# Kernel tuning notes

Measured on AMD Instinct MI355X. Metric: run time of the kernel, lower is better.

## Reference

```python
import jax, jax.numpy as jnp
from jax import lax
import numpy as np

BATCH = 8
FH, FW, A = 32, 256, 6            # feature map height/width, anchors per cell
TOTAL_ANCHORS = FH * FW * A       # 49152
PRE_NMS_TOPN = 2000
POST_NMS_TOPN = 300
NMS_IOU = 0.7
VARIANCES = np.array([0.1, 0.1, 0.2, 0.2], dtype=np.float32)


def _make_anchors():
    # Grid anchors, normalized [y1, x1, y2, x2], A scales/ratios per cell.
    cy = (np.arange(FH, dtype=np.float32) + 0.5) / FH
    cx = (np.arange(FW, dtype=np.float32) + 0.5) / FW
    sizes = np.array([0.02, 0.04, 0.08, 0.03, 0.06, 0.12], dtype=np.float32)  # A sizes
    ratios = np.array([1.0, 1.0, 1.0, 2.0, 0.5, 1.0], dtype=np.float32)
    h = sizes * np.sqrt(ratios)
    w = sizes / np.sqrt(ratios)
    CY, CX = np.meshgrid(cy, cx, indexing='ij')            # [FH, FW]
    CY = CY[:, :, None]; CX = CX[:, :, None]               # [FH, FW, 1]
    y1 = CY - 0.5 * h; x1 = CX - 0.5 * w
    y2 = CY + 0.5 * h; x2 = CX + 0.5 * w
    anc = np.stack([y1, x1, y2, x2], axis=-1).reshape(-1, 4)  # [TOTAL_ANCHORS, 4]
    return jnp.asarray(anc, dtype=jnp.float32)


def setup_inputs() -> dict:
    key = jax.random.key(0)
    k1, k2 = jax.random.split(key)
    rpn_bbox_deltas = jax.random.normal(k1, (BATCH, FH, FW, A * 4), dtype=jnp.float32)
    rpn_labels = jax.random.normal(k2, (BATCH, FH, FW, A), dtype=jnp.float32)
    return {
        'rpn_bbox_deltas': rpn_bbox_deltas,
        'rpn_labels': rpn_labels,
        'anchors': _make_anchors(),
    }


def _decode(anchors, deltas):
    # anchors [N,4] y1x1y2x2, deltas [B,N,4] (dy,dx,dh,dw)
    ah = anchors[:, 2] - anchors[:, 0]
    aw = anchors[:, 3] - anchors[:, 1]
    acy = anchors[:, 0] + 0.5 * ah
    acx = anchors[:, 1] + 0.5 * aw
    bh = jnp.exp(deltas[..., 2]) * ah
    bw = jnp.exp(deltas[..., 3]) * aw
    bcy = deltas[..., 0] * ah + acy
    bcx = deltas[..., 1] * aw + acx
    y1 = bcy - 0.5 * bh
    x1 = bcx - 0.5 * bw
    return jnp.stack([y1, x1, y1 + bh, x1 + bw], axis=-1)


def _pairwise_iou(boxes):
    # boxes [N,4] -> [N,N]
    y1, x1, y2, x2 = boxes[:, 0], boxes[:, 1], boxes[:, 2], boxes[:, 3]
    area = (y2 - y1) * (x2 - x1)
    iy1 = jnp.maximum(y1[:, None], y1[None, :])
    ix1 = jnp.maximum(x1[:, None], x1[None, :])
    iy2 = jnp.minimum(y2[:, None], y2[None, :])
    ix2 = jnp.minimum(x2[:, None], x2[None, :])
    inter = jnp.maximum(iy2 - iy1, 0.0) * jnp.maximum(ix2 - ix1, 0.0)
    union = area[:, None] + area[None, :] - inter
    return inter / jnp.maximum(union, 1e-8)


def _nms_single(boxes, scores):
    # boxes [P,4] sorted by score desc, scores [P] in [0,1]
    P = boxes.shape[0]
    ious = _pairwise_iou(boxes)
    idx = jnp.arange(P)

    def body(i, keep):
        sup = (ious[i] > NMS_IOU) & (idx > i) & keep[i]
        return keep & (~sup)

    keep = lax.fori_loop(0, P, body, jnp.ones((P,), dtype=bool))
    masked = jnp.where(keep, scores, -1.0)
    top_sc, top_idx = lax.top_k(masked, POST_NMS_TOPN)
    valid = top_sc >= 0.0
    out_boxes = jnp.clip(boxes[top_idx], 0.0, 1.0) * valid[:, None].astype(boxes.dtype)
    out_scores = jnp.where(valid, top_sc, 0.0)
    return out_boxes, out_scores


def reference(rpn_bbox_deltas, rpn_labels, anchors):
    B = rpn_bbox_deltas.shape[0]
    deltas = rpn_bbox_deltas.reshape(B, TOTAL_ANCHORS, 4)
    labels = jax.nn.softmax(rpn_labels, axis=-1).reshape(B, TOTAL_ANCHORS)
    deltas = deltas * jnp.asarray(VARIANCES)
    bboxes = _decode(anchors, deltas)                          # [B, N, 4]
    pre_scores, pre_idx = lax.top_k(labels, PRE_NMS_TOPN)      # [B, P]
    pre_boxes = jnp.take_along_axis(bboxes, pre_idx[:, :, None], axis=1)  # [B, P, 4]
    roi_boxes, roi_scores = jax.vmap(_nms_single)(pre_boxes, pre_scores)
    return (lax.stop_gradient(roi_boxes), lax.stop_gradient(roi_scores))
```

## Files before the change

kernel.cpp:

```cpp
#include <hip/hip_runtime.h>
#include <cstdint>
#include <cstddef>

#define BATCH 8
#define FHh   32
#define FWw   256
#define NA    6
#define NANCH (FHh * FWw * NA)
#define PRE_K 2000
#define POST_K 300
#define SEGS  192
#define CAND_CAP 4096
#define BIN_LO 0x3E2Au
#define SH_BASE 0x3E00u
#define SHBIN 512
#define RMAX_EP 20

typedef unsigned long long u64;

#define WS_SC   0
#define WS_HIST 1572864
#define WS_CAND 4194304
#define WS_CNT  7340032
#define WS_PB   7602176
#define WS_PS   7858176
#define WS_SUPP 8388608

__global__ __launch_bounds__(1024) void k_zero(uint4* __restrict__ hist4) {
    hist4[threadIdx.x] = make_uint4(0u, 0u, 0u, 0u);
}

__global__ void k_softhist(const float* __restrict__ labels, float* __restrict__ scores,
                           unsigned int* __restrict__ hist) {
    int pos = blockIdx.x * blockDim.x + threadIdx.x;
    if (pos >= BATCH * FHh * FWw) return;
    int b = pos / (FHh * FWw);
    const float2* in2 = (const float2*)(labels + (size_t)pos * NA);
    float v[NA];
    float2 p0 = in2[0], p1 = in2[1], p2 = in2[2];
    v[0] = p0.x; v[1] = p0.y; v[2] = p1.x; v[3] = p1.y; v[4] = p2.x; v[5] = p2.y;
    float m = v[0];
#pragma unroll
    for (int a = 1; a < NA; ++a) m = fmaxf(m, v[a]);
    float s = 0.0f;
#pragma unroll
    for (int a = 0; a < NA; ++a) { v[a] = expf(v[a] - m); s += v[a]; }
    float inv = 1.0f / s;
    float2* o2 = (float2*)(scores + (size_t)pos * NA);
    unsigned int* hb = hist + (size_t)b * SHBIN;
#pragma unroll
    for (int a = 0; a < NA; ++a) v[a] *= inv;
    o2[0] = make_float2(v[0], v[1]);
    o2[1] = make_float2(v[2], v[3]);
    o2[2] = make_float2(v[4], v[5]);
#pragma unroll
    for (int a = 0; a < NA; ++a) {
        unsigned int bin = __float_as_uint(v[a]) >> 16;
        if (bin >= BIN_LO) atomicAdd(&hb[bin - SH_BASE], 1u);
    }
}

__global__ __launch_bounds__(256) void k_gather(
        const float* __restrict__ scores, const unsigned int* __restrict__ hist,
        u64* __restrict__ cand, unsigned int* __restrict__ counts) {
    const int blk = blockIdx.x;
    const int b = blk / SEGS, kb = blk - b * SEGS;
    const int tid = threadIdx.x;
    const int lane = tid & 63, w = tid >> 6;
    __shared__ unsigned int s_wsum[4];
    __shared__ unsigned int s_cut;
    __shared__ unsigned int s_wcnt[4];

    const unsigned int* hb = hist + (size_t)b * SHBIN;
    const int base = SHBIN - 2 * (tid + 1);
    unsigned int hlo = hb[base], hhi = hb[base + 1];
    unsigned int s = hlo + hhi;
    unsigned int inc = s;
#pragma unroll
    for (int d = 1; d < 64; d <<= 1) {
        unsigned int v = __shfl_up(inc, d);
        if (lane >= d) inc += v;
    }
    if (lane == 63) s_wsum[w] = inc;
    __syncthreads();
    unsigned int woff = 0;
#pragma unroll
    for (int i = 0; i < 4; ++i) if (i < w) woff += s_wsum[i];
    unsigned int excl = woff + inc - s;
    if (excl < PRE_K && excl + s >= PRE_K) {
        unsigned int run = excl + hhi;
        s_cut = SH_BASE + (unsigned int)(run >= PRE_K ? base + 1 : base);
    }
    __syncthreads();
    const unsigned int cutr = s_cut;

    const int idx = kb * 256 + tid;
    const unsigned int bits = __float_as_uint(scores[(size_t)b * NANCH + idx]);
    const bool pass = (bits >> 16) >= cutr;
    const u64 m = __ballot(pass);
    if (lane == 0) s_wcnt[w] = (unsigned int)__popcll(m);
    __syncthreads();
    unsigned int pre = 0, tot = 0;
#pragma unroll
    for (int i = 0; i < 4; ++i) { unsigned int c = s_wcnt[i]; if (i < w) pre += c; tot += c; }
    if (pass) {
        unsigned int rank = pre + (unsigned int)__popcll(m & ((1ull << lane) - 1ull));
        cand[((size_t)b * SEGS + kb) * 256 + rank] =
            ((u64)bits << 32) | (unsigned int)(~idx);
    }
    if (tid == 0) counts[b * SEGS + kb] = tot;
}

__global__ __launch_bounds__(1024) void k_rankdec(
        const u64* __restrict__ cand, const unsigned int* __restrict__ counts,
        const unsigned int* __restrict__ hist,
        const float* __restrict__ deltas, const float* __restrict__ anchors,
        float4* __restrict__ pre_boxes, float* __restrict__ pre_scores) {
    const int b = blockIdx.x;
    const int tid = threadIdx.x;
    const int lane = tid & 63, wid = tid >> 6;
    __shared__ u64 grouped[CAND_CAP];
    __shared__ unsigned int cursor[CAND_CAP];
    __shared__ unsigned int sfx_lds[SHBIN];
    __shared__ unsigned int s_ws8[8];
    for (int i = tid; i < CAND_CAP; i += 1024) { grouped[i] = 0ull; cursor[i] = 0u; }

    unsigned int c = (tid < SHBIN) ? hist[(size_t)b * SHBIN + (SHBIN - 1 - tid)] : 0u;
    unsigned int inc = c;
#pragma unroll
    for (int d = 1; d < 64; d <<= 1) {
        unsigned int v = __shfl_up(inc, d);
        if (lane >= d) inc += v;
    }
    if (lane == 63 && wid < 8) s_ws8[wid] = inc;
    __syncthreads();
    if (tid < SHBIN) {
        unsigned int woff = 0;
#pragma unroll
        for (int i = 0; i < 8; ++i) if (i < wid) woff += s_ws8[i];
        sfx_lds[SHBIN - 1 - tid] = woff + inc - c;
    }
    __syncthreads();

    if (tid < SEGS) {
        unsigned int v = counts[b * SEGS + tid];
        const u64* seg = cand + ((size_t)b * SEGS + tid) * 256;
        for (unsigned int k = 0; k < v; ++k) {
            u64 key = seg[k];
            unsigned int bin = (unsigned int)(key >> 48) - SH_BASE;
            unsigned int g0 = sfx_lds[bin];
            unsigned int slot = g0 + atomicAdd(&cursor[g0], 1u);
            if (slot < CAND_CAP) grouped[slot] = key;
        }
    }
    __syncthreads();

    for (int p = tid; p < CAND_CAP; p += 1024) {
        u64 key = grouped[p];
        if (key == 0ull) continue;
        unsigned int bin = (unsigned int)(key >> 48) - SH_BASE;
        unsigned int g0 = sfx_lds[bin];
        unsigned int cg = cursor[g0];
        unsigned int rank = g0;
        unsigned int qe = g0 + cg; if (qe > CAND_CAP) qe = CAND_CAP;
        for (unsigned int q = g0; q < qe; ++q) rank += (grouped[q] > key);
        if (rank < PRE_K) {
            int idx = (int)(~(unsigned int)key);
            float score = __uint_as_float((unsigned int)(key >> 32));
            const float* anc = anchors + (size_t)idx * 4;
            const float* del = deltas + ((size_t)b * NANCH + idx) * 4;
            float a0 = anc[0], a1 = anc[1], a2 = anc[2], a3 = anc[3];
            float ah = a2 - a0, aw = a3 - a1;
            float acy = a0 + 0.5f * ah, acx = a1 + 0.5f * aw;
            float d0 = del[0] * 0.1f, d1 = del[1] * 0.1f;
            float d2 = del[2] * 0.2f, d3 = del[3] * 0.2f;
            float bh = expf(d2) * ah, bw = expf(d3) * aw;
            float bcy = d0 * ah + acy, bcx = d1 * aw + acx;
            float y1 = bcy - 0.5f * bh, x1 = bcx - 0.5f * bw;
            pre_boxes[(size_t)b * PRE_K + rank] = make_float4(y1, x1, y1 + bh, x1 + bw);
            pre_scores[(size_t)b * PRE_K + rank] = score;
        }
    }
}

__global__ __launch_bounds__(64) void k_iou(const float4* __restrict__ pre_boxes,
                                            u64* __restrict__ supp) {
    const int cb = blockIdx.x;
    const int rb = blockIdx.y;
    const int b  = blockIdx.z;
    const int lane = threadIdx.x;
    const int i = rb * 64 + lane;
    const int j0 = cb * 64;
    if (cb < rb) return;
    __shared__ float4 sbox[64];
    const float4* boxes = pre_boxes + (size_t)b * PRE_K;
    int j = j0 + lane;
    sbox[lane] = (j < PRE_K) ? boxes[j] : make_float4(0.f, 0.f, 0.f, 0.f);
    __syncthreads();
    if (i >= PRE_K) return;
    float4 bi = boxes[i];
    float area_i = (bi.z - bi.x) * (bi.w - bi.y);
    u64 bits = 0ull;
    const int tmax = (PRE_K - j0 < 64) ? (PRE_K - j0) : 64;
    for (int t = 0; t < tmax; ++t) {
        int jj = j0 + t;
        if (jj <= i) continue;
        float4 bj = sbox[t];
        float iy1 = fmaxf(bi.x, bj.x), ix1 = fmaxf(bi.y, bj.y);
        float iy2 = fminf(bi.z, bj.z), ix2 = fminf(bi.w, bj.w);
        float inter = fmaxf(iy2 - iy1, 0.0f) * fmaxf(ix2 - ix1, 0.0f);
        float area_j = (bj.z - bj.x) * (bj.w - bj.y);
        float uni = area_i + area_j - inter;
        float iou = inter / fmaxf(uni, 1e-8f);
        if (iou > 0.7f) bits |= (1ull << t);
    }
    supp[((size_t)b * PRE_K + i) * 32 + cb] = bits;
}

__device__ __forceinline__ u64 readlane64(u64 x, int ln) {
    unsigned int lo = __builtin_amdgcn_readlane((unsigned int)x, ln);
    unsigned int hi = __builtin_amdgcn_readlane((unsigned int)(x >> 32), ln);
    return ((u64)hi << 32) | (u64)lo;
}

template <int ROWS>
__device__ __forceinline__ u64 proc_epoch(const u64* __restrict__ bufp, int wi,
                                          int p, int w, u64& r0, u64& r1) {
    const u64 wmask = (w >= wi) ? ~0ull : 0ull;
    u64 acc = r0 | r1;
    u64 cur = ~(readlane64(acc, wi) | readlane64(acc, 32 + wi));
#pragma unroll
    for (int g = 0; g < ROWS / 16; ++g) {
        u64 ld[8];
#pragma unroll
        for (int k = 0; k < 8; ++k)
            ld[k] = bufp[(g * 16 + 2 * k + p) * 32 + w] & wmask;
        u64 t0 = (ld[0] | ld[1]) | (ld[2] | ld[3]);
        u64 t1 = (ld[4] | ld[5]) | (ld[6] | ld[7]);
        u64 tor = t0 | t1;
        u64 intra = readlane64(tor, wi) | readlane64(tor, 32 + wi);
        if (intra == 0ull) {
#pragma unroll
            for (int k = 0; k < 8; ++k) {
                int bitpos = g * 16 + 2 * k + p;
                u64 msk = ((cur >> bitpos) & 1ull) ? ~0ull : 0ull;
                if (k & 1) r1 |= ld[k] & msk; else r0 |= ld[k] & msk;
            }
        } else {
#pragma unroll
            for (int c = 0; c < 16; ++c) {
                const int pi = c & 1, k = c >> 1;
                if ((cur >> (g * 16 + c)) & 1ull) {
                    cur &= ~readlane64(ld[k], pi * 32 + wi);
                    u64 msk = (p == pi) ? ~0ull : 0ull;
                    if (k & 1) r1 |= ld[k] & msk; else r0 |= ld[k] & msk;
                }
            }
        }
    }
    return cur;
}

__device__ void fill_epoch(u64* __restrict__ dst, const float4* __restrict__ boxes,
                           int e, int l, int rows) {
    const int total = rows * 32;
    for (int idx = l; idx < total; idx += 64) {
        const int rl = idx >> 5, w = idx & 31;
        const int i = e * 64 + rl;
        const int j0 = w * 64;
        u64 bits = 0ull;
        if (i < PRE_K && j0 + 63 > i) {
            float4 bi = boxes[i];
            float area_i = (bi.z - bi.x) * (bi.w - bi.y);
            const int tmax = (PRE_K - j0 < 64) ? (PRE_K - j0) : 64;
            for (int t = 0; t < tmax; ++t) {
                int jj = j0 + t;
                if (jj <= i) continue;
                float4 bj = boxes[jj];
                float iy1 = fmaxf(bi.x, bj.x), ix1 = fmaxf(bi.y, bj.y);
                float iy2 = fminf(bi.z, bj.z), ix2 = fminf(bi.w, bj.w);
                float inter = fmaxf(iy2 - iy1, 0.0f) * fmaxf(ix2 - ix1, 0.0f);
                float area_j = (bj.z - bj.x) * (bj.w - bj.y);
                float uni = area_i + area_j - inter;
                float iou = inter / fmaxf(uni, 1e-8f);
                if (iou > 0.7f) bits |= (1ull << t);
            }
        }
        dst[idx] = bits;
    }
}

__global__ __launch_bounds__(64) void k_final(const u64* __restrict__ supp,
                        const float4* __restrict__ pre_boxes,
                        const float* __restrict__ pre_scores,
                        float* __restrict__ out) {
    const int b = blockIdx.x;
    const int l = threadIdx.x;
    const int p = l >> 5, w = l & 31;
    float* ob = out + (size_t)b * POST_K * 4;
    float* os = out + (size_t)BATCH * POST_K * 4 + (size_t)b * POST_K;
    for (int t = l; t < POST_K * 4; t += 64) ob[t] = 0.0f;
    for (int t = l; t < POST_K; t += 64) os[t] = 0.0f;
    asm volatile("s_waitcnt vmcnt(0)" ::: "memory");

    __shared__ u64 sbuf[5][2048];
    const char* Sb = (const char*)(supp + (size_t)b * PRE_K * 32);
    const float4* boxes = pre_boxes + (size_t)b * PRE_K;

#define ISSUE_EPOCH(ep)                                                       \
    do {                                                                      \
        const char* gsrc_ = Sb + (size_t)(ep) * 16384 + (size_t)l * 16;       \
        char* ldst_ = (char*)&sbuf[(ep) % 5][0];                              \
        _Pragma("unroll")                                                     \
        for (int k_ = 0; k_ < 16; ++k_)                                       \
            __builtin_amdgcn_global_load_lds(                                 \
                (const __attribute__((address_space(1))) void*)(gsrc_ + k_ * 1024), \
                (__attribute__((address_space(3))) void*)(ldst_ + k_ * 1024), \
                16, 0, 0);                                                    \
    } while (0)

    u64 r0 = 0ull, r1 = 0ull;
    int kept = 0;
    bool done = false;
    ISSUE_EPOCH(0);
    ISSUE_EPOCH(1);
    ISSUE_EPOCH(2);
    ISSUE_EPOCH(3);
    for (int e = 0; e < RMAX_EP; ++e) {
        if (e <= RMAX_EP - 4)      asm volatile("s_waitcnt vmcnt(48)" ::: "memory");
        else if (e == RMAX_EP - 3) asm volatile("s_waitcnt vmcnt(32)" ::: "memory");
        else if (e == RMAX_EP - 2) asm volatile("s_waitcnt vmcnt(16)" ::: "memory");
        else                       asm volatile("s_waitcnt vmcnt(0)"  ::: "memory");
        __builtin_amdgcn_sched_barrier(0);
        if (e + 4 < RMAX_EP) ISSUE_EPOCH(e + 4);
        u64 curf = proc_epoch<64>(&sbuf[e % 5][0], e, p, w, r0, r1);
        kept += __builtin_popcountll(curf);
        if (kept >= POST_K) { done = true; break; }
    }
    asm volatile("s_waitcnt vmcnt(0)" ::: "memory");
    if (!done) {
        for (int e = RMAX_EP; e < 32; ++e) {
            fill_epoch(&sbuf[0][0], boxes, e, l, (e == 31) ? 16 : 64);
            __syncthreads();
            u64 curf;
            if (e < 31) curf = proc_epoch<64>(&sbuf[0][0], e, p, w, r0, r1);
            else        curf = proc_epoch<16>(&sbuf[0][0], e, p, w, r0, r1) & 0xFFFFull;
            kept += __builtin_popcountll(curf);
            if (kept >= POST_K) break;
            __syncthreads();
        }
    }
#undef ISSUE_EPOCH

    u64 full = r0 | r1;
    u64 oth = __shfl(full, w + 32);
    u64 kw = ~(full | oth);
    if (w == 31) kw &= 0xFFFFull;
    int cnt = (l < 32) ? __builtin_popcountll(kw) : 0;
    int cum = cnt;
#pragma unroll
    for (int d = 1; d < 64; d <<= 1) {
        int v = __shfl_up(cum, d);
        if (l >= d) cum += v;
    }
    int r = cum - cnt;
    __syncthreads();
    if (l < 32) {
        u64 m = kw;
        while (m != 0ull && r < POST_K) {
            int t = __builtin_ctzll(m);
            m &= m - 1ull;
            int i = w * 64 + t;
            float4 bx = pre_boxes[(size_t)b * PRE_K + i];
            ob[r * 4 + 0] = fminf(fmaxf(bx.x, 0.0f), 1.0f);
            ob[r * 4 + 1] = fminf(fmaxf(bx.y, 0.0f), 1.0f);
            ob[r * 4 + 2] = fminf(fmaxf(bx.z, 0.0f), 1.0f);
            ob[r * 4 + 3] = fminf(fmaxf(bx.w, 0.0f), 1.0f);
            os[r] = pre_scores[(size_t)b * PRE_K + i];
            ++r;
        }
    }
}

extern "C" void kernel_launch(void* const* d_in, const int* in_sizes, int n_in,
                              void* d_out, int out_size, void* d_ws, size_t ws_size,
                              hipStream_t stream) {
    const float* deltas  = (const float*)d_in[0];
    const float* labels  = (const float*)d_in[1];
    const float* anchors = (const float*)d_in[2];
    float* out = (float*)d_out;

    char* ws = (char*)d_ws;
    float* scores          = (float*)(ws + WS_SC);
    unsigned int* hist     = (unsigned int*)(ws + WS_HIST);
    u64* cd                = (u64*)(ws + WS_CAND);
    unsigned int* cntp     = (unsigned int*)(ws + WS_CNT);
    float4* pre_boxes      = (float4*)(ws + WS_PB);
    float* pre_scores      = (float*)(ws + WS_PS);
    u64* sp                = (u64*)(ws + WS_SUPP);

    k_zero<<<1, 1024, 0, stream>>>((uint4*)hist);
    k_softhist<<<(BATCH * FHh * FWw + 255) / 256, 256, 0, stream>>>(labels, scores, hist);
    k_gather<<<BATCH * SEGS, 256, 0, stream>>>(scores, hist, cd, cntp);
    k_rankdec<<<BATCH, 1024, 0, stream>>>(cd, cntp, hist, deltas, anchors,
                                          pre_boxes, pre_scores);
    k_iou<<<dim3(32, RMAX_EP, BATCH), 64, 0, stream>>>(pre_boxes, sp);
    k_final<<<BATCH, 64, 0, stream>>>(sp, pre_boxes, pre_scores, out);
}
```

Baseline: 87.13 us.

## Warp-specialize NMS final kernel with producer waves streaming suppression epochs

Expands k_final from one wavefront to eight. Wave 0 runs the serial NMS scan, and seven producer waves load suppression-mask epochs into an eight-deep LDS ring, signalling readiness through workgroup-scope atomic flags. The fallback IoU fill for late epochs now uses all 512 threads. The aim is to take memory latency off the serial scan, at the cost of spin-wait polling and more LDS per block.

```diff
diff --git a/kernel.cpp b/kernel.cpp
--- a/kernel.cpp
+++ b/kernel.cpp
@@ -15,6 +15,7 @@
 #define SH_BASE 0x3E00u
 #define SHBIN 512
 #define RMAX_EP 20
+#define NBUF 8
 
 typedef unsigned long long u64;
 
@@ -262,9 +263,9 @@
 }
 
 __device__ void fill_epoch(u64* __restrict__ dst, const float4* __restrict__ boxes,
-                           int e, int l, int rows) {
+                           int e, int l, int nthreads, int rows) {
     const int total = rows * 32;
-    for (int idx = l; idx < total; idx += 64) {
+    for (int idx = l; idx < total; idx += nthreads) {
         const int rl = idx >> 5, w = idx & 31;
         const int i = e * 64 + rl;
         const int j0 = w * 64;
@@ -290,94 +291,117 @@
     }
 }
 
-__global__ __launch_bounds__(64) void k_final(const u64* __restrict__ supp,
+#define LDS_LD(p)  __hip_atomic_load((p), __ATOMIC_ACQUIRE, __HIP_MEMORY_SCOPE_WORKGROUP)
+#define LDS_ST(p, v) __hip_atomic_store((p), (v), __ATOMIC_RELEASE, __HIP_MEMORY_SCOPE_WORKGROUP)
+
+__global__ __launch_bounds__(512) void k_final(const u64* __restrict__ supp,
                         const float4* __restrict__ pre_boxes,
                         const float* __restrict__ pre_scores,
                         float* __restrict__ out) {
     const int b = blockIdx.x;
     const int l = threadIdx.x;
-    const int p = l >> 5, w = l & 31;
+    const int wv = l >> 6;
+    const int lw = l & 63;
+    const int p = lw >> 5, w = lw & 31;
     float* ob = out + (size_t)b * POST_K * 4;
     float* os = out + (size_t)BATCH * POST_K * 4 + (size_t)b * POST_K;
-    for (int t = l; t < POST_K * 4; t += 64) ob[t] = 0.0f;
-    for (int t = l; t < POST_K; t += 64) os[t] = 0.0f;
-    asm volatile("s_waitcnt vmcnt(0)" ::: "memory");
-
-    __shared__ u64 sbuf[5][2048];
+    for (int t = l; t < POST_K * 4; t += 512) ob[t] = 0.0f;
+    for (int t = l; t < POST_K; t += 512) os[t] = 0.0f;
+
+    __shared__ u64 sbuf[NBUF][2048];
+    __shared__ int s_ready[RMAX_EP];
+    __shared__ int s_consumed;
+    __shared__ int s_abort;
+    __shared__ int s_done;
+    __shared__ int s_kept;
+    if (l < RMAX_EP) s_ready[l] = 0;
+    if (l == 0) { s_consumed = 0; s_abort = 0; s_done = 0; s_kept = 0; }
+    __syncthreads();
+
     const char* Sb = (const char*)(supp + (size_t)b * PRE_K * 32);
     const float4* boxes = pre_boxes + (size_t)b * PRE_K;
 
-#define ISSUE_EPOCH(ep)                                                       \
-    do {                                                                      \
-        const char* gsrc_ = Sb + (size_t)(ep) * 16384 + (size_t)l * 16;       \
-        char* ldst_ = (char*)&sbuf[(ep) % 5][0];                              \
-        _Pragma("unroll")                                                     \
-        for (int k_ = 0; k_ < 16; ++k_)                                       \
-            __builtin_amdgcn_global_load_lds(                                 \
-                (const __attribute__((address_space(1))) void*)(gsrc_ + k_ * 1024), \
-                (__attribute__((address_space(3))) void*)(ldst_ + k_ * 1024), \
-                16, 0, 0);                                                    \
-    } while (0)
-
     u64 r0 = 0ull, r1 = 0ull;
     int kept = 0;
-    bool done = false;
-    ISSUE_EPOCH(0);
-    ISSUE_EPOCH(1);
-    ISSUE_EPOCH(2);
-    ISSUE_EPOCH(3);
-    for (int e = 0; e < RMAX_EP; ++e) {
-        if (e <= RMAX_EP - 4)      asm volatile("s_waitcnt vmcnt(48)" ::: "memory");
-        else if (e == RMAX_EP - 3) asm volatile("s_waitcnt vmcnt(32)" ::: "memory");
-        else if (e == RMAX_EP - 2) asm volatile("s_waitcnt vmcnt(16)" ::: "memory");
-        else                       asm volatile("s_waitcnt vmcnt(0)"  ::: "memory");
-        __builtin_amdgcn_sched_barrier(0);
-        if (e + 4 < RMAX_EP) ISSUE_EPOCH(e + 4);
-        u64 curf = proc_epoch<64>(&sbuf[e % 5][0], e, p, w, r0, r1);
-        kept += __builtin_popcountll(curf);
-        if (kept >= POST_K) { done = true; break; }
-    }
-    asm volatile("s_waitcnt vmcnt(0)" ::: "memory");
-    if (!done) {
-        for (int e = RMAX_EP; e < 32; ++e) {
-            fill_epoch(&sbuf[0][0], boxes, e, l, (e == 31) ? 16 : 64);
-            __syncthreads();
+
+    if (wv == 0) {
+        for (int e = 0; e < RMAX_EP; ++e) {
+            while (LDS_LD(&s_ready[e]) == 0) __builtin_amdgcn_s_sleep(2);
+            __builtin_amdgcn_sched_barrier(0);
+            u64 curf = proc_epoch<64>(&sbuf[e % NBUF][0], e, p, w, r0, r1);
+            kept += __builtin_popcountll(curf);
+            LDS_ST(&s_consumed, e + 1);
+            if (kept >= POST_K) break;
+        }
+        if (lw == 0) {
+            s_kept = kept;
+            if (kept >= POST_K) s_done = 1;
+            LDS_ST(&s_abort, 1);
+        }
+    } else {
+        for (int e = wv - 1; e < RMAX_EP; e += 7) {
+            bool bail = false;
+            while (LDS_LD(&s_consumed) < e - (NBUF - 1)) {
+                if (LDS_LD(&s_abort)) { bail = true; break; }
+                __builtin_amdgcn_s_sleep(2);
+            }
+            if (bail || LDS_LD(&s_abort)) break;
+            const char* gsrc = Sb + (size_t)e * 16384 + (size_t)lw * 16;
+            char* ldst = (char*)&sbuf[e % NBUF][0];
+#pragma unroll
+            for (int k = 0; k < 16; ++k)
+                __builtin_amdgcn_global_load_lds(
+                    (const __attribute__((address_space(1))) void*)(gsrc + k * 1024),
+                    (__attribute__((address_space(3))) void*)(ldst + lw * 16 + k * 1024),
+                    16, 0, 0);
+            asm volatile("s_waitcnt vmcnt(0)" ::: "memory");
+            if (lw == 0) LDS_ST(&s_ready[e], 1);
+        }
+    }
+    __syncthreads();
+    kept = s_kept;
+
+    for (int e = RMAX_EP; e < 32; ++e) {
+        if (s_done) break;
+        fill_epoch(&sbuf[0][0], boxes, e, l, 512, (e == 31) ? 16 : 64);
+        __syncthreads();
+        if (wv == 0) {
             u64 curf;
             if (e < 31) curf = proc_epoch<64>(&sbuf[0][0], e, p, w, r0, r1);
             else        curf = proc_epoch<16>(&sbuf[0][0], e, p, w, r0, r1) & 0xFFFFull;
             kept += __builtin_popcountll(curf);
-            if (kept >= POST_K) break;
-            __syncthreads();
-        }
-    }
-#undef ISSUE_EPOCH
-
-    u64 full = r0 | r1;
-    u64 oth = __shfl(full, w + 32);
-    u64 kw = ~(full | oth);
-    if (w == 31) kw &= 0xFFFFull;
-    int cnt = (l < 32) ? __builtin_popcountll(kw) : 0;
-    int cum = cnt;
-#pragma unroll
-    for (int d = 1; d < 64; d <<= 1) {
-        int v = __shfl_up(cum, d);
-        if (l >= d) cum += v;
-    }
-    int r = cum - cnt;
-    __syncthreads();
-    if (l < 32) {
-        u64 m = kw;
-        while (m != 0ull && r < POST_K) {
-            int t = __builtin_ctzll(m);
-            m &= m - 1ull;
-            int i = w * 64 + t;
-            float4 bx = pre_boxes[(size_t)b * PRE_K + i];
-            ob[r * 4 + 0] = fminf(fmaxf(bx.x, 0.0f), 1.0f);
-            ob[r * 4 + 1] = fminf(fmaxf(bx.y, 0.0f), 1.0f);
-            ob[r * 4 + 2] = fminf(fmaxf(bx.z, 0.0f), 1.0f);
-            ob[r * 4 + 3] = fminf(fmaxf(bx.w, 0.0f), 1.0f);
-            os[r] = pre_scores[(size_t)b * PRE_K + i];
-            ++r;
+            if (lw == 0 && kept >= POST_K) s_done = 1;
+        }
+        __syncthreads();
+    }
+
+    if (wv == 0) {
+        u64 full = r0 | r1;
+        u64 oth = __shfl(full, w + 32);
+        u64 kw = ~(full | oth);
+        if (w == 31) kw &= 0xFFFFull;
+        int cnt = (lw < 32) ? __builtin_popcountll(kw) : 0;
+        int cum = cnt;
+#pragma unroll
+        for (int d = 1; d < 64; d <<= 1) {
+            int v = __shfl_up(cum, d);
+            if (lw >= d) cum += v;
+        }
+        int r = cum - cnt;
+        if (lw < 32) {
+            u64 m = kw;
+            while (m != 0ull && r < POST_K) {
+                int t = __builtin_ctzll(m);
+                m &= m - 1ull;
+                int i = w * 64 + t;
+                float4 bx = pre_boxes[(size_t)b * PRE_K + i];
+                ob[r * 4 + 0] = fminf(fmaxf(bx.x, 0.0f), 1.0f);
+                ob[r * 4 + 1] = fminf(fmaxf(bx.y, 0.0f), 1.0f);
+                ob[r * 4 + 2] = fminf(fmaxf(bx.z, 0.0f), 1.0f);
+                ob[r * 4 + 3] = fminf(fmaxf(bx.w, 0.0f), 1.0f);
+                os[r] = pre_scores[(size_t)b * PRE_K + i];
+                ++r;
+            }
         }
     }
 }
@@ -405,5 +429,5 @@
     k_rankdec<<<BATCH, 1024, 0, stream>>>(cd, cntp, hist, deltas, anchors,
                                           pre_boxes, pre_scores);
     k_iou<<<dim3(32, RMAX_EP, BATCH), 64, 0, stream>>>(pre_boxes, sp);
-    k_final<<<BATCH, 64, 0, stream>>>(sp, pre_boxes, pre_scores, out);
-}
+    k_final<<<BATCH, 512, 0, stream>>>(sp, pre_boxes, pre_scores, out);
+}
```

Result: no change. 86.79 us (-0.4%).

## Fuse IoU and NMS kernels with per-epoch counters; privatize softmax histogram

Applied to the files above, without the earlier changes.

Merges the pairwise-IoU kernel and the final NMS kernel into one launch. Blocks 0..BATCH-1 run the sequential NMS scan and spin on per-epoch atomic counters that the IoU blocks bump after writing their bitmask rows, so the scan can start on early epochs while later IoU tiles are still being computed. The LDS ring shrinks from 5 to 3 buffers. Separately, the softmax/histogram kernel now accumulates into a shared-memory histogram and flushes it with one global atomic per nonzero bin instead of one global atomic per score. This risks deadlock if the NMS blocks are scheduled before the IoU blocks and the IoU blocks cannot be placed. It also adds polling and fence overhead.

```diff
diff --git a/kernel.cpp b/kernel.cpp
--- a/kernel.cpp
+++ b/kernel.cpp
@@ -24,17 +24,26 @@
 #define WS_CNT  7340032
 #define WS_PB   7602176
 #define WS_PS   7858176
+#define WS_EPC  7922176
 #define WS_SUPP 8388608
 
-__global__ __launch_bounds__(1024) void k_zero(uint4* __restrict__ hist4) {
+__global__ __launch_bounds__(1024) void k_zero(uint4* __restrict__ hist4,
+                                               unsigned int* __restrict__ epc) {
     hist4[threadIdx.x] = make_uint4(0u, 0u, 0u, 0u);
-}
-
-__global__ void k_softhist(const float* __restrict__ labels, float* __restrict__ scores,
-                           unsigned int* __restrict__ hist) {
-    int pos = blockIdx.x * blockDim.x + threadIdx.x;
-    if (pos >= BATCH * FHh * FWw) return;
-    int b = pos / (FHh * FWw);
+    if (threadIdx.x < BATCH * RMAX_EP) epc[threadIdx.x] = 0u;
+}
+
+__global__ __launch_bounds__(256) void k_softhist(
+        const float* __restrict__ labels, float* __restrict__ scores,
+        unsigned int* __restrict__ hist) {
+    const int blk = blockIdx.x;
+    const int b = blk >> 5;
+    const int tid = threadIdx.x;
+    __shared__ unsigned int lh[SHBIN];
+    lh[tid] = 0u; lh[tid + 256] = 0u;
+    __syncthreads();
+
+    const int pos = blk * 256 + tid;
     const float2* in2 = (const float2*)(labels + (size_t)pos * NA);
     float v[NA];
     float2 p0 = in2[0], p1 = in2[1], p2 = in2[2];
@@ -47,7 +56,6 @@
     for (int a = 0; a < NA; ++a) { v[a] = expf(v[a] - m); s += v[a]; }
     float inv = 1.0f / s;
     float2* o2 = (float2*)(scores + (size_t)pos * NA);
-    unsigned int* hb = hist + (size_t)b * SHBIN;
 #pragma unroll
     for (int a = 0; a < NA; ++a) v[a] *= inv;
     o2[0] = make_float2(v[0], v[1]);
@@ -56,8 +64,14 @@
 #pragma unroll
     for (int a = 0; a < NA; ++a) {
         unsigned int bin = __float_as_uint(v[a]) >> 16;
-        if (bin >= BIN_LO) atomicAdd(&hb[bin - SH_BASE], 1u);
-    }
+        if (bin >= BIN_LO) atomicAdd(&lh[bin - SH_BASE], 1u);
+    }
+    __syncthreads();
+    unsigned int* hb = hist + (size_t)b * SHBIN;
+    unsigned int c0 = lh[tid];
+    unsigned int c1 = lh[tid + 256];
+    if (c0) atomicAdd(&hb[tid], c0);
+    if (c1) atomicAdd(&hb[tid + 256], c1);
 }
 
 __global__ __launch_bounds__(256) void k_gather(
@@ -183,40 +197,6 @@
     }
 }
 
-__global__ __launch_bounds__(64) void k_iou(const float4* __restrict__ pre_boxes,
-                                            u64* __restrict__ supp) {
-    const int cb = blockIdx.x;
-    const int rb = blockIdx.y;
-    const int b  = blockIdx.z;
-    const int lane = threadIdx.x;
-    const int i = rb * 64 + lane;
-    const int j0 = cb * 64;
-    if (cb < rb) return;
-    __shared__ float4 sbox[64];
-    const float4* boxes = pre_boxes + (size_t)b * PRE_K;
-    int j = j0 + lane;
-    sbox[lane] = (j < PRE_K) ? boxes[j] : make_float4(0.f, 0.f, 0.f, 0.f);
-    __syncthreads();
-    if (i >= PRE_K) return;
-    float4 bi = boxes[i];
-    float area_i = (bi.z - bi.x) * (bi.w - bi.y);
-    u64 bits = 0ull;
-    const int tmax = (PRE_K - j0 < 64) ? (PRE_K - j0) : 64;
-    for (int t = 0; t < tmax; ++t) {
-        int jj = j0 + t;
-        if (jj <= i) continue;
-        float4 bj = sbox[t];
-        float iy1 = fmaxf(bi.x, bj.x), ix1 = fmaxf(bi.y, bj.y);
-        float iy2 = fminf(bi.z, bj.z), ix2 = fminf(bi.w, bj.w);
-        float inter = fmaxf(iy2 - iy1, 0.0f) * fmaxf(ix2 - ix1, 0.0f);
-        float area_j = (bj.z - bj.x) * (bj.w - bj.y);
-        float uni = area_i + area_j - inter;
-        float iou = inter / fmaxf(uni, 1e-8f);
-        if (iou > 0.7f) bits |= (1ull << t);
-    }
-    supp[((size_t)b * PRE_K + i) * 32 + cb] = bits;
-}
-
 __device__ __forceinline__ u64 readlane64(u64 x, int ln) {
     unsigned int lo = __builtin_amdgcn_readlane((unsigned int)x, ln);
     unsigned int hi = __builtin_amdgcn_readlane((unsigned int)(x >> 32), ln);
@@ -262,9 +242,9 @@
 }
 
 __device__ void fill_epoch(u64* __restrict__ dst, const float4* __restrict__ boxes,
-                           int e, int l, int rows) {
+                           int e, int l, int nthreads, int rows) {
     const int total = rows * 32;
-    for (int idx = l; idx < total; idx += 64) {
+    for (int idx = l; idx < total; idx += nthreads) {
         const int rl = idx >> 5, w = idx & 31;
         const int i = e * 64 + rl;
         const int j0 = w * 64;
@@ -290,12 +270,55 @@
     }
 }
 
-__global__ __launch_bounds__(64) void k_final(const u64* __restrict__ supp,
-                        const float4* __restrict__ pre_boxes,
-                        const float* __restrict__ pre_scores,
-                        float* __restrict__ out) {
-    const int b = blockIdx.x;
+#define EPC_LD(p) __hip_atomic_load((p), __ATOMIC_ACQUIRE, __HIP_MEMORY_SCOPE_AGENT)
+
+__global__ __launch_bounds__(64) void k_ioufinal(
+        const float4* __restrict__ pre_boxes, const float* __restrict__ pre_scores,
+        u64* __restrict__ supp, unsigned int* __restrict__ epcnt,
+        float* __restrict__ out) {
+    const int blk = blockIdx.x;
     const int l = threadIdx.x;
+    __shared__ u64 sbuf[3][2048];
+
+    if (blk >= BATCH) {
+        const int rem = blk - BATCH;
+        const int b = rem / (RMAX_EP * 32);
+        const int r2 = rem - b * (RMAX_EP * 32);
+        const int rb = r2 >> 5, cb = r2 & 31;
+        const float4* boxes = pre_boxes + (size_t)b * PRE_K;
+        if (cb >= rb) {
+            float4* sbox = (float4*)&sbuf[0][0];
+            const int i = rb * 64 + l;
+            const int j0 = cb * 64;
+            int j = j0 + l;
+            sbox[l] = (j < PRE_K) ? boxes[j] : make_float4(0.f, 0.f, 0.f, 0.f);
+            __syncthreads();
+            if (i < PRE_K) {
+                float4 bi = boxes[i];
+                float area_i = (bi.z - bi.x) * (bi.w - bi.y);
+                u64 bits = 0ull;
+                const int tmax = (PRE_K - j0 < 64) ? (PRE_K - j0) : 64;
+                for (int t = 0; t < tmax; ++t) {
+                    int jj = j0 + t;
+                    if (jj <= i) continue;
+                    float4 bj = sbox[t];
+                    float iy1 = fmaxf(bi.x, bj.x), ix1 = fmaxf(bi.y, bj.y);
+                    float iy2 = fminf(bi.z, bj.z), ix2 = fminf(bi.w, bj.w);
+                    float inter = fmaxf(iy2 - iy1, 0.0f) * fmaxf(ix2 - ix1, 0.0f);
+                    float area_j = (bj.z - bj.x) * (bj.w - bj.y);
+                    float uni = area_i + area_j - inter;
+                    float iou = inter / fmaxf(uni, 1e-8f);
+                    if (iou > 0.7f) bits |= (1ull << t);
+                }
+                supp[((size_t)b * PRE_K + i) * 32 + cb] = bits;
+            }
+        }
+        __threadfence();
+        if (l == 0) atomicAdd(&epcnt[b * RMAX_EP + rb], 1u);
+        return;
+    }
+
+    const int b = blk;
     const int p = l >> 5, w = l & 31;
     float* ob = out + (size_t)b * POST_K * 4;
     float* os = out + (size_t)BATCH * POST_K * 4 + (size_t)b * POST_K;
@@ -303,14 +326,14 @@
     for (int t = l; t < POST_K; t += 64) os[t] = 0.0f;
     asm volatile("s_waitcnt vmcnt(0)" ::: "memory");
 
-    __shared__ u64 sbuf[5][2048];
     const char* Sb = (const char*)(supp + (size_t)b * PRE_K * 32);
     const float4* boxes = pre_boxes + (size_t)b * PRE_K;
+    const unsigned int* ec = &epcnt[b * RMAX_EP];
 
 #define ISSUE_EPOCH(ep)                                                       \
     do {                                                                      \
         const char* gsrc_ = Sb + (size_t)(ep) * 16384 + (size_t)l * 16;       \
-        char* ldst_ = (char*)&sbuf[(ep) % 5][0];                              \
+        char* ldst_ = (char*)&sbuf[(ep) % 3][0];                              \
         _Pragma("unroll")                                                     \
         for (int k_ = 0; k_ < 16; ++k_)                                       \
             __builtin_amdgcn_global_load_lds(                                 \
@@ -320,27 +343,29 @@
     } while (0)
 
     u64 r0 = 0ull, r1 = 0ull;
-    int kept = 0;
+    int kept = 0, issued = 0;
     bool done = false;
-    ISSUE_EPOCH(0);
-    ISSUE_EPOCH(1);
-    ISSUE_EPOCH(2);
-    ISSUE_EPOCH(3);
-    for (int e = 0; e < RMAX_EP; ++e) {
-        if (e <= RMAX_EP - 4)      asm volatile("s_waitcnt vmcnt(48)" ::: "memory");
-        else if (e == RMAX_EP - 3) asm volatile("s_waitcnt vmcnt(32)" ::: "memory");
-        else if (e == RMAX_EP - 2) asm volatile("s_waitcnt vmcnt(16)" ::: "memory");
-        else                       asm volatile("s_waitcnt vmcnt(0)"  ::: "memory");
+    for (int e = 0; e < RMAX_EP && !done; ++e) {
+        while (issued <= e) {
+            while (EPC_LD(&ec[issued]) < 32u) __builtin_amdgcn_s_sleep(8);
+            ISSUE_EPOCH(issued); ++issued;
+        }
+        while (issued < RMAX_EP && issued < e + 3 && EPC_LD(&ec[issued]) >= 32u) {
+            ISSUE_EPOCH(issued); ++issued;
+        }
+        const int lag = issued - 1 - e;
+        if (lag <= 0)      asm volatile("s_waitcnt vmcnt(0)"  ::: "memory");
+        else if (lag == 1) asm volatile("s_waitcnt vmcnt(16)" ::: "memory");
+        else               asm volatile("s_waitcnt vmcnt(32)" ::: "memory");
         __builtin_amdgcn_sched_barrier(0);
-        if (e + 4 < RMAX_EP) ISSUE_EPOCH(e + 4);
-        u64 curf = proc_epoch<64>(&sbuf[e % 5][0], e, p, w, r0, r1);
+        u64 curf = proc_epoch<64>(&sbuf[e % 3][0], e, p, w, r0, r1);
         kept += __builtin_popcountll(curf);
-        if (kept >= POST_K) { done = true; break; }
+        if (kept >= POST_K) done = true;
     }
     asm volatile("s_waitcnt vmcnt(0)" ::: "memory");
     if (!done) {
         for (int e = RMAX_EP; e < 32; ++e) {
-            fill_epoch(&sbuf[0][0], boxes, e, l, (e == 31) ? 16 : 64);
+            fill_epoch(&sbuf[0][0], boxes, e, l, 64, (e == 31) ? 16 : 64);
             __syncthreads();
             u64 curf;
             if (e < 31) curf = proc_epoch<64>(&sbuf[0][0], e, p, w, r0, r1);
@@ -364,7 +389,6 @@
         if (l >= d) cum += v;
     }
     int r = cum - cnt;
-    __syncthreads();
     if (l < 32) {
         u64 m = kw;
         while (m != 0ull && r < POST_K) {
@@ -397,13 +421,14 @@
     unsigned int* cntp     = (unsigned int*)(ws + WS_CNT);
     float4* pre_boxes      = (float4*)(ws + WS_PB);
     float* pre_scores      = (float*)(ws + WS_PS);
+    unsigned int* epc      = (unsigned int*)(ws + WS_EPC);
     u64* sp                = (u64*)(ws + WS_SUPP);
 
-    k_zero<<<1, 1024, 0, stream>>>((uint4*)hist);
-    k_softhist<<<(BATCH * FHh * FWw + 255) / 256, 256, 0, stream>>>(labels, scores, hist);
+    k_zero<<<1, 1024, 0, stream>>>((uint4*)hist, epc);
+    k_softhist<<<256, 256, 0, stream>>>(labels, scores, hist);
     k_gather<<<BATCH * SEGS, 256, 0, stream>>>(scores, hist, cd, cntp);
     k_rankdec<<<BATCH, 1024, 0, stream>>>(cd, cntp, hist, deltas, anchors,
                                           pre_boxes, pre_scores);
-    k_iou<<<dim3(32, RMAX_EP, BATCH), 64, 0, stream>>>(pre_boxes, sp);
-    k_final<<<BATCH, 64, 0, stream>>>(sp, pre_boxes, pre_scores, out);
-}
+    k_ioufinal<<<BATCH + BATCH * RMAX_EP * 32, 64, 0, stream>>>(
+        pre_boxes, pre_scores, sp, epc, out);
+}
```

Measured after the change: 214.6 us. 146% more time.
